# Optimization experiments

Measured on AMD Instinct MI355X. Metric: run time of the kernel, lower is better.

Reference implementation:

```python
import jax, jax.numpy as jnp
import numpy as np

D_MODEL = 1024
N_HEADS = 16
HEAD_DIM = D_MODEL // N_HEADS


def setup_inputs() -> dict:
    key = jax.random.key(0)
    ks = jax.random.split(key, 5)
    B, S = 2, 2048
    x = jax.random.normal(ks[0], (B, S, D_MODEL), dtype=jnp.float32)
    # nn.Linear weights: [out_features, in_features]
    s_in = 1.0 / np.sqrt(D_MODEL)
    qkv_w = jax.random.uniform(ks[1], (3 * D_MODEL, D_MODEL), jnp.float32, -s_in, s_in)
    qkv_b = jax.random.uniform(ks[2], (3 * D_MODEL,), jnp.float32, -s_in, s_in)
    out_w = jax.random.uniform(ks[3], (D_MODEL, D_MODEL), jnp.float32, -s_in, s_in)
    out_b = jax.random.uniform(ks[4], (D_MODEL,), jnp.float32, -s_in, s_in)
    return {"x": x, "qkv_w": qkv_w, "qkv_b": qkv_b, "out_w": out_w, "out_b": out_b}


def reference(x, qkv_w, qkv_b, out_w, out_b):
    B, S, D = x.shape
    H, Hd = N_HEADS, HEAD_DIM
    scale = 1.0 / np.sqrt(Hd)
    qkv = jnp.einsum('bsd,ed->bse', x, qkv_w) + qkv_b  # [B,S,3D]
    qkv = qkv.reshape(B, S, 3, H, Hd)
    q = qkv[:, :, 0].transpose(0, 2, 1, 3)  # [B,H,S,Hd]
    k = qkv[:, :, 1].transpose(0, 2, 1, 3)
    v = qkv[:, :, 2].transpose(0, 2, 1, 3)
    scores = jnp.einsum('bhqd,bhkd->bhqk', q, k) * scale  # [B,H,S,S]
    causal = jnp.triu(jnp.ones((S, S), dtype=bool), k=1)
    scores = jnp.where(causal[None, None], -jnp.inf, scores)
    probs = jax.nn.softmax(scores, axis=-1)
    out = jnp.einsum('bhqk,bhkd->bhqd', probs, v)  # [B,H,S,Hd]
    out = out.transpose(0, 2, 1, 3).reshape(B, S, D)
    out = jnp.einsum('bsd,ed->bse', out, out_w) + out_b
    return out
```

## Files before the change

### kernel.cpp

```cpp
#include <hip/hip_runtime.h>
#include <hip/hip_bf16.h>

#define SEQ    2048
#define DMODEL 1024
#define NHEAD  16
#define HDIM   64
#define BATCH  2
#define NTOK   (BATCH * SEQ)

#define N_X   (NTOK * DMODEL)
#define N_WQ  (3 * DMODEL * DMODEL)
#define N_BQ  (3 * DMODEL)
#define N_WO  (DMODEL * DMODEL)
#define N_BO  (DMODEL)
#define N_CANON (N_X + N_WQ + N_BQ + N_WO + N_BO)

#define NEG_SENT (-1.0e30f)
#define QSCALE 0.1803368801111f

typedef __attribute__((ext_vector_type(8))) short short8;
typedef __attribute__((ext_vector_type(4))) short short4v;
typedef __attribute__((ext_vector_type(4))) float f32x4;

#define MFMA_BF16(A, B, C) __builtin_amdgcn_mfma_f32_16x16x32_bf16((A), (B), (C), 0, 0, 0)

static __device__ __forceinline__ short8 load8(const __hip_bfloat16* p) {
    return *(const short8*)p;
}

static __device__ __forceinline__ void async16(const void* g, void* l) {
    __builtin_amdgcn_global_load_lds(
        (const __attribute__((address_space(1))) unsigned int*)g,
        (__attribute__((address_space(3))) unsigned int*)l,
        16, 0, 0);
}

__global__ void detect_kernel(const unsigned short* __restrict__ w, int* flag) {
    int cnt = 0;
    for (int i = threadIdx.x; i < 512; i += 64) {
        const unsigned e = (w[i] >> 7) & 0xFF;
        if (e >= 125) cnt++;
    }
#pragma unroll
    for (int o = 32; o; o >>= 1) cnt += __shfl_down(cnt, o);
    if (threadIdx.x == 0) *flag = (cnt > 8) ? 1 : 0;
}

__global__ __launch_bounds__(256) void canon_kernel(
    const void* __restrict__ s0, const void* __restrict__ s1,
    const void* __restrict__ s2, const void* __restrict__ s3,
    const void* __restrict__ s4,
    __hip_bfloat16* __restrict__ dst, const int* __restrict__ flag)
{
    const int idx = blockIdx.x * 256 + threadIdx.x;
    if (idx >= N_CANON) return;
    const void* src;
    int off;
    if (idx < N_X)                         { src = s0; off = idx; }
    else if (idx < N_X + N_WQ)             { src = s1; off = idx - N_X; }
    else if (idx < N_X + N_WQ + N_BQ)      { src = s2; off = idx - (N_X + N_WQ); }
    else if (idx < N_X + N_WQ + N_BQ + N_WO){ src = s3; off = idx - (N_X + N_WQ + N_BQ); }
    else                                   { src = s4; off = idx - (N_X + N_WQ + N_BQ + N_WO); }
    const bool isf32 = (*flag != 0);
    const float v = isf32 ? ((const float*)src)[off]
                          : __bfloat162float(((const __hip_bfloat16*)src)[off]);
    dst[idx] = __float2bfloat16(v);
}

__global__ __launch_bounds__(256) void qkv_gemm_kernel(
    const __hip_bfloat16* __restrict__ X,
    const __hip_bfloat16* __restrict__ W,
    const __hip_bfloat16* __restrict__ bias,
    __hip_bfloat16* __restrict__ Qs,
    __hip_bfloat16* __restrict__ Kb,
    __hip_bfloat16* __restrict__ Vt)
{
    constexpr int Kd = DMODEL;
    __shared__ __align__(16) __hip_bfloat16 As[128 * 32];
    __shared__ __align__(16) __hip_bfloat16 Bs[128 * 32];

    const int tid   = threadIdx.x;
    const int lane  = tid & 63;
    const int w     = tid >> 6;
    const int mTile = blockIdx.y * 128;
    const int nTile = blockIdx.x * 128;
    const int wm    = (w >> 1) * 64;
    const int wn    = (w & 1) * 64;
    const int lm    = lane & 15;
    const int lk    = (lane >> 4) * 8;

    f32x4 acc[4][4];
#pragma unroll
    for (int i = 0; i < 4; ++i)
#pragma unroll
        for (int j = 0; j < 4; ++j)
            acc[i][j] = (f32x4){0.f, 0.f, 0.f, 0.f};

    const int r0c = tid >> 2, p0c = tid & 3;
    const int r1c = (tid + 256) >> 2, p1c = tid & 3;

    for (int k0 = 0; k0 < Kd; k0 += 32) {
        __syncthreads();
        async16(&X[(size_t)(mTile + r0c) * Kd + k0 + p0c * 8], (char*)As + tid * 16);
        async16(&X[(size_t)(mTile + r1c) * Kd + k0 + p1c * 8], (char*)As + tid * 16 + 4096);
        async16(&W[(size_t)(nTile + r0c) * Kd + k0 + p0c * 8], (char*)Bs + tid * 16);
        async16(&W[(size_t)(nTile + r1c) * Kd + k0 + p1c * 8], (char*)Bs + tid * 16 + 4096);
        __syncthreads();

        short8 a[4], b[4];
#pragma unroll
        for (int i = 0; i < 4; ++i)
            a[i] = *(const short8*)&As[(wm + i * 16 + lm) * 32 + lk];
#pragma unroll
        for (int j = 0; j < 4; ++j)
            b[j] = *(const short8*)&Bs[(wn + j * 16 + lm) * 32 + lk];
#pragma unroll
        for (int i = 0; i < 4; ++i)
#pragma unroll
            for (int j = 0; j < 4; ++j)
                acc[i][j] = MFMA_BF16(a[i], b[j], acc[i][j]);
    }

    const int r0 = (lane >> 4) * 4;
#pragma unroll
    for (int j = 0; j < 4; ++j) {
        const int n  = nTile + wn + j * 16 + lm;
        const float bv = __bfloat162float(bias[n]);
        const int c = n >> 10;
        const int h = (n >> 6) & 15;
        const int d = n & 63;
#pragma unroll
        for (int i = 0; i < 4; ++i) {
#pragma unroll
            for (int r = 0; r < 4; ++r) {
                const int m  = mTile + wm + i * 16 + r0 + r;
                const int bb = m >> 11;
                const int s  = m & (SEQ - 1);
                const int bh = bb * NHEAD + h;
                const float v = acc[i][j][r] + bv;
                if (c == 0) {
                    Qs[(size_t)(bh * SEQ + s) * HDIM + d] = __float2bfloat16(v * QSCALE);
                } else if (c == 1) {
                    Kb[(size_t)(bh * SEQ + s) * HDIM + d] = __float2bfloat16(v);
                } else {
                    Vt[(size_t)(bh * HDIM + d) * SEQ + s] = __float2bfloat16(v);
                }
            }
        }
    }
}

#define P_PITCH 72
__global__ __launch_bounds__(256, 2) void attn_kernel(
    const __hip_bfloat16* __restrict__ Qs,
    const __hip_bfloat16* __restrict__ Kb,
    const __hip_bfloat16* __restrict__ Vt,
    __hip_bfloat16* __restrict__ O)
{
    __shared__ __align__(16) __hip_bfloat16 Kt[64 * 64];
    __shared__ __align__(16) __hip_bfloat16 Vs[64 * 64];
    __shared__ __align__(16) __hip_bfloat16 Pall[4][32 * P_PITCH];

    const int lane = threadIdx.x & 63;
    const int wv   = threadIdx.x >> 6;
    const int pr   = blockIdx.x;
    const int bh   = blockIdx.y;

    const int lm  = lane & 15;
    const int q4  = lane >> 4;
    const int lk  = q4 * 8;
    const int swz = (lm & 3) << 4;

    __hip_bfloat16* P = Pall[wv];

    const __hip_bfloat16* Qbh = Qs + (size_t)bh * SEQ * HDIM;
    const __hip_bfloat16* Kbh = Kb + (size_t)bh * SEQ * HDIM;
    const __hip_bfloat16* Vbh = Vt + (size_t)bh * HDIM * SEQ;

    const int srow = (lane >> 3);
    const int scb  = (lane & 7) ^ srow;
    const int krow0 = wv * 16 + srow;
    const int krow1 = wv * 16 + 8 + srow;

    const int b  = bh >> 4;
    const int hh = bh & 15;

    for (int ph = 0; ph < 2; ++ph) {
        const int qb    = ph ? pr : 15 - pr;
        const int qbase = qb * 128;
        const int wbase = qbase + wv * 32;

        short8 qa[2][2];
#pragma unroll
        for (int i = 0; i < 2; ++i)
#pragma unroll
            for (int h = 0; h < 2; ++h)
                qa[i][h] = load8(&Qbh[(size_t)(wbase + i * 16 + lm) * HDIM + h * 32 + lk]);

        float m_run[2] = {NEG_SENT, NEG_SENT};
        float l_run[2] = {0.f, 0.f};
        f32x4 Oacc[2][4];
#pragma unroll
        for (int i = 0; i < 2; ++i)
#pragma unroll
            for (int t = 0; t < 4; ++t) Oacc[i][t] = (f32x4){0.f, 0.f, 0.f, 0.f};

        const int nChunks = 2 * (qb + 1);
        for (int c = 0; c < nChunks; ++c) {
            const int k0 = c * 64;

            __syncthreads();
            async16(&Kbh[(size_t)(k0 + krow0) * HDIM + scb * 8],
                    (char*)Kt + (size_t)(wv * 16) * 128 + (lane * 16));
            async16(&Kbh[(size_t)(k0 + krow1) * HDIM + scb * 8],
                    (char*)Kt + (size_t)(wv * 16 + 8) * 128 + (lane * 16));
            async16(&Vbh[(size_t)krow0 * SEQ + k0 + scb * 8],
                    (char*)Vs + (size_t)(wv * 16) * 128 + (lane * 16));
            async16(&Vbh[(size_t)krow1 * SEQ + k0 + scb * 8],
                    (char*)Vs + (size_t)(wv * 16 + 8) * 128 + (lane * 16));
            __syncthreads();

            if (k0 <= wbase + 31) {
                short8 ka[4][2];
#pragma unroll
                for (int t = 0; t < 4; ++t)
#pragma unroll
                    for (int h = 0; h < 2; ++h)
                        ka[t][h] = *(const short8*)&Kt[(t * 16 + lm) * 64 +
                                                       (((h * 4 + q4) ^ (lm & 7)) * 8)];

                f32x4 sc[2][4];
#pragma unroll
                for (int i = 0; i < 2; ++i)
#pragma unroll
                    for (int t = 0; t < 4; ++t) sc[i][t] = (f32x4){0.f, 0.f, 0.f, 0.f};
#pragma unroll
                for (int t = 0; t < 4; ++t)
#pragma unroll
                    for (int i = 0; i < 2; ++i) {
                        sc[i][t] = MFMA_BF16(ka[t][0], qa[i][0], sc[i][t]);
                        sc[i][t] = MFMA_BF16(ka[t][1], qa[i][1], sc[i][t]);
                    }

                if (k0 + 63 > wbase) {
#pragma unroll
                    for (int i = 0; i < 2; ++i) {
                        const int row = wbase + i * 16 + lm;
#pragma unroll
                        for (int t = 0; t < 4; ++t)
#pragma unroll
                            for (int r = 0; r < 4; ++r) {
                                const int key = k0 + t * 16 + q4 * 4 + r;
                                if (key > row) sc[i][t][r] = NEG_SENT;
                            }
                    }
                }

                float alpha[2];
#pragma unroll
                for (int i = 0; i < 2; ++i) {
                    float mx = sc[i][0][0];
#pragma unroll
                    for (int t = 0; t < 4; ++t)
#pragma unroll
                        for (int r = 0; r < 4; ++r) mx = fmaxf(mx, sc[i][t][r]);
                    mx = fmaxf(mx, __shfl_xor(mx, 16));
                    mx = fmaxf(mx, __shfl_xor(mx, 32));
                    const float mn = fmaxf(m_run[i], mx);
                    alpha[i] = exp2f(m_run[i] - mn);
                    float s = 0.f;
#pragma unroll
                    for (int t = 0; t < 4; ++t)
#pragma unroll
                        for (int r = 0; r < 4; ++r) {
                            const float p = exp2f(sc[i][t][r] - mn);
                            sc[i][t][r] = p;
                            s += p;
                        }
                    s += __shfl_xor(s, 16);
                    s += __shfl_xor(s, 32);
                    l_run[i] = l_run[i] * alpha[i] + s;
                    m_run[i] = mn;
                }

#pragma unroll
                for (int i = 0; i < 2; ++i)
#pragma unroll
                    for (int r = 0; r < 4; ++r) {
                        const float av = __shfl(alpha[i], q4 * 4 + r);
#pragma unroll
                        for (int t = 0; t < 4; ++t) Oacc[i][t][r] *= av;
                    }

#pragma unroll
                for (int i = 0; i < 2; ++i)
#pragma unroll
                    for (int t = 0; t < 4; ++t) {
                        short4v pk;
#pragma unroll
                        for (int r = 0; r < 4; ++r)
                            pk[r] = (short)__bfloat16_as_ushort(__float2bfloat16(sc[i][t][r]));
                        const int col = (t * 16 + q4 * 4) ^ swz;
                        *(short4v*)&P[(i * 16 + lm) * P_PITCH + col] = pk;
                    }

#pragma unroll
                for (int h = 0; h < 2; ++h) {
                    short8 pa[2];
#pragma unroll
                    for (int i = 0; i < 2; ++i) {
                        const int col = (h * 32 + lk) ^ swz;
                        pa[i] = *(const short8*)&P[(i * 16 + lm) * P_PITCH + col];
                    }
#pragma unroll
                    for (int t = 0; t < 4; ++t) {
                        const short8 vb = *(const short8*)&Vs[(t * 16 + lm) * 64 +
                                                              (((h * 4 + q4) ^ (lm & 7)) * 8)];
#pragma unroll
                        for (int i = 0; i < 2; ++i)
                            Oacc[i][t] = MFMA_BF16(pa[i], vb, Oacc[i][t]);
                    }
                }
            }
        }

#pragma unroll
        for (int i = 0; i < 2; ++i)
#pragma unroll
            for (int r = 0; r < 4; ++r) {
                const float lv = __shfl(l_run[i], q4 * 4 + r);
                const float inv = 1.0f / lv;
                const size_t m = (size_t)b * SEQ + wbase + i * 16 + q4 * 4 + r;
#pragma unroll
                for (int t = 0; t < 4; ++t)
                    O[m * DMODEL + hh * 64 + t * 16 + lm] = __float2bfloat16(Oacc[i][t][r] * inv);
            }
    }
}

__global__ __launch_bounds__(256) void proj_gemm_kernel(
    const __hip_bfloat16* __restrict__ A,
    const __hip_bfloat16* __restrict__ W,
    const __hip_bfloat16* __restrict__ bias,
    void* __restrict__ outv,
    const int* __restrict__ flag)
{
    constexpr int Kd = DMODEL;
    __shared__ __align__(16) __hip_bfloat16 As[128 * 32];
    __shared__ __align__(16) __hip_bfloat16 Bs[128 * 32];

    const int tid   = threadIdx.x;
    const int lane  = tid & 63;
    const int w     = tid >> 6;
    const int mTile = blockIdx.y * 128;
    const int nTile = blockIdx.x * 128;
    const int wm    = (w >> 1) * 64;
    const int wn    = (w & 1) * 64;
    const int lm    = lane & 15;
    const int lk    = (lane >> 4) * 8;
    const bool f32out = (*flag != 0);

    f32x4 acc[4][4];
#pragma unroll
    for (int i = 0; i < 4; ++i)
#pragma unroll
        for (int j = 0; j < 4; ++j)
            acc[i][j] = (f32x4){0.f, 0.f, 0.f, 0.f};

    const int r0c = tid >> 2, p0c = tid & 3;
    const int r1c = (tid + 256) >> 2, p1c = tid & 3;

    for (int k0 = 0; k0 < Kd; k0 += 32) {
        __syncthreads();
        async16(&A[(size_t)(mTile + r0c) * Kd + k0 + p0c * 8], (char*)As + tid * 16);
        async16(&A[(size_t)(mTile + r1c) * Kd + k0 + p1c * 8], (char*)As + tid * 16 + 4096);
        async16(&W[(size_t)(nTile + r0c) * Kd + k0 + p0c * 8], (char*)Bs + tid * 16);
        async16(&W[(size_t)(nTile + r1c) * Kd + k0 + p1c * 8], (char*)Bs + tid * 16 + 4096);
        __syncthreads();

        short8 a[4], b[4];
#pragma unroll
        for (int i = 0; i < 4; ++i)
            a[i] = *(const short8*)&As[(wm + i * 16 + lm) * 32 + lk];
#pragma unroll
        for (int j = 0; j < 4; ++j)
            b[j] = *(const short8*)&Bs[(wn + j * 16 + lm) * 32 + lk];
#pragma unroll
        for (int i = 0; i < 4; ++i)
#pragma unroll
            for (int j = 0; j < 4; ++j)
                acc[i][j] = MFMA_BF16(a[i], b[j], acc[i][j]);
    }

    const int r0 = (lane >> 4) * 4;
#pragma unroll
    for (int j = 0; j < 4; ++j) {
        const int n = nTile + wn + j * 16 + lm;
        const float bv = __bfloat162float(bias[n]);
#pragma unroll
        for (int i = 0; i < 4; ++i) {
#pragma unroll
            for (int r = 0; r < 4; ++r) {
                const size_t m = mTile + wm + i * 16 + r0 + r;
                const float v = acc[i][j][r] + bv;
                if (f32out) ((float*)outv)[m * DMODEL + n] = v;
                else ((__hip_bfloat16*)outv)[m * DMODEL + n] = __float2bfloat16(v);
            }
        }
    }
}

extern "C" void kernel_launch(void* const* d_in, const int* in_sizes, int n_in,
                              void* d_out, int out_size, void* d_ws, size_t ws_size,
                              hipStream_t stream) {
    const size_t OFF_CANON = 256;
    const size_t OFF_QS = OFF_CANON + (size_t)N_CANON * 2;
    const size_t OFF_KB = OFF_QS + (size_t)NTOK * DMODEL * 2;
    const size_t OFF_VT = OFF_KB + (size_t)NTOK * DMODEL * 2;
    const size_t OFF_AO = OFF_VT + (size_t)NTOK * DMODEL * 2;

    char* wsb = (char*)d_ws;
    int* flag = (int*)wsb;
    __hip_bfloat16* canon = (__hip_bfloat16*)(wsb + OFF_CANON);
    __hip_bfloat16* Xc = canon;
    __hip_bfloat16* Wq = Xc + N_X;
    __hip_bfloat16* Bq = Wq + N_WQ;
    __hip_bfloat16* Wo = Bq + N_BQ;
    __hip_bfloat16* Bo = Wo + N_WO;
    __hip_bfloat16* Qs = (__hip_bfloat16*)(wsb + OFF_QS);
    __hip_bfloat16* Kb = (__hip_bfloat16*)(wsb + OFF_KB);
    __hip_bfloat16* Vt = (__hip_bfloat16*)(wsb + OFF_VT);
    __hip_bfloat16* Ao = (__hip_bfloat16*)(wsb + OFF_AO);

    detect_kernel<<<1, 64, 0, stream>>>((const unsigned short*)d_in[1], flag);
    canon_kernel<<<(N_CANON + 255) / 256, 256, 0, stream>>>(
        d_in[0], d_in[1], d_in[2], d_in[3], d_in[4], canon, flag);

    {
        dim3 grid(3 * DMODEL / 128, NTOK / 128);
        qkv_gemm_kernel<<<grid, 256, 0, stream>>>(Xc, Wq, Bq, Qs, Kb, Vt);
    }
    {
        dim3 grid(8, BATCH * NHEAD);
        attn_kernel<<<grid, 256, 0, stream>>>(Qs, Kb, Vt, Ao);
    }
    {
        dim3 grid(DMODEL / 128, NTOK / 128);
        proj_gemm_kernel<<<grid, 256, 0, stream>>>(Ao, Wo, Bo, d_out, flag);
    }
}
```

Baseline: 232.4 us.

## Double-buffer K/V tiles and split attention block into eight 16-row waves

The attention kernel now runs 512 threads (8 waves), each wave handling 16 query rows instead of 32. K/V tiles are double-buffered in shared memory, with the next chunk's async loads issued before computing on the current one, using explicit vmcnt waits and raw barriers. This is meant to hide global-load latency and raise wave-level parallelism. In exchange, each wave reuses its K/V fragments across fewer rows, shared memory use grows, and the hand-written waitcnt and barrier sequencing adds fragility.

```diff
diff --git a/kernel.cpp b/kernel.cpp
--- a/kernel.cpp
+++ b/kernel.cpp
@@ -151,18 +151,19 @@
 }
 
 #define P_PITCH 72
-__global__ __launch_bounds__(256, 2) void attn_kernel(
+__global__ __launch_bounds__(512, 2) void attn_kernel(
     const __hip_bfloat16* __restrict__ Qs,
     const __hip_bfloat16* __restrict__ Kb,
     const __hip_bfloat16* __restrict__ Vt,
     __hip_bfloat16* __restrict__ O)
 {
-    __shared__ __align__(16) __hip_bfloat16 Kt[64 * 64];
-    __shared__ __align__(16) __hip_bfloat16 Vs[64 * 64];
-    __shared__ __align__(16) __hip_bfloat16 Pall[4][32 * P_PITCH];
-
-    const int lane = threadIdx.x & 63;
-    const int wv   = threadIdx.x >> 6;
+    __shared__ __align__(16) __hip_bfloat16 Kt[2][64 * 64];
+    __shared__ __align__(16) __hip_bfloat16 Vs[2][64 * 64];
+    __shared__ __align__(16) __hip_bfloat16 Pall[8][16 * P_PITCH];
+
+    const int tid  = threadIdx.x;
+    const int lane = tid & 63;
+    const int wv   = tid >> 6;
     const int pr   = blockIdx.x;
     const int bh   = blockIdx.y;
 
@@ -177,164 +178,146 @@
     const __hip_bfloat16* Kbh = Kb + (size_t)bh * SEQ * HDIM;
     const __hip_bfloat16* Vbh = Vt + (size_t)bh * HDIM * SEQ;
 
-    const int srow = (lane >> 3);
-    const int scb  = (lane & 7) ^ srow;
-    const int krow0 = wv * 16 + srow;
-    const int krow1 = wv * 16 + 8 + srow;
+    const int srow = tid >> 3;
+    const int scb  = (tid & 7) ^ (srow & 7);
 
     const int b  = bh >> 4;
     const int hh = bh & 15;
 
     for (int ph = 0; ph < 2; ++ph) {
         const int qb    = ph ? pr : 15 - pr;
-        const int qbase = qb * 128;
-        const int wbase = qbase + wv * 32;
-
-        short8 qa[2][2];
-#pragma unroll
-        for (int i = 0; i < 2; ++i)
-#pragma unroll
-            for (int h = 0; h < 2; ++h)
-                qa[i][h] = load8(&Qbh[(size_t)(wbase + i * 16 + lm) * HDIM + h * 32 + lk]);
-
-        float m_run[2] = {NEG_SENT, NEG_SENT};
-        float l_run[2] = {0.f, 0.f};
-        f32x4 Oacc[2][4];
-#pragma unroll
-        for (int i = 0; i < 2; ++i)
-#pragma unroll
-            for (int t = 0; t < 4; ++t) Oacc[i][t] = (f32x4){0.f, 0.f, 0.f, 0.f};
+        const int wbase = qb * 128 + wv * 16;
+
+        short8 qa[2];
+#pragma unroll
+        for (int h = 0; h < 2; ++h)
+            qa[h] = load8(&Qbh[(size_t)(wbase + lm) * HDIM + h * 32 + lk]);
+
+        float m_run = NEG_SENT;
+        float l_run = 0.f;
+        f32x4 Oacc[4];
+#pragma unroll
+        for (int t = 0; t < 4; ++t) Oacc[t] = (f32x4){0.f, 0.f, 0.f, 0.f};
 
         const int nChunks = 2 * (qb + 1);
+        int cur = 0;
+
+        async16(&Kbh[(size_t)srow * HDIM + scb * 8], (char*)Kt[0] + tid * 16);
+        async16(&Vbh[(size_t)srow * SEQ + scb * 8],  (char*)Vs[0] + tid * 16);
+
         for (int c = 0; c < nChunks; ++c) {
             const int k0 = c * 64;
 
-            __syncthreads();
-            async16(&Kbh[(size_t)(k0 + krow0) * HDIM + scb * 8],
-                    (char*)Kt + (size_t)(wv * 16) * 128 + (lane * 16));
-            async16(&Kbh[(size_t)(k0 + krow1) * HDIM + scb * 8],
-                    (char*)Kt + (size_t)(wv * 16 + 8) * 128 + (lane * 16));
-            async16(&Vbh[(size_t)krow0 * SEQ + k0 + scb * 8],
-                    (char*)Vs + (size_t)(wv * 16) * 128 + (lane * 16));
-            async16(&Vbh[(size_t)krow1 * SEQ + k0 + scb * 8],
-                    (char*)Vs + (size_t)(wv * 16 + 8) * 128 + (lane * 16));
-            __syncthreads();
-
-            if (k0 <= wbase + 31) {
+            if (c + 1 < nChunks) {
+                const int k1 = k0 + 64;
+                async16(&Kbh[(size_t)(k1 + srow) * HDIM + scb * 8],
+                        (char*)Kt[cur ^ 1] + tid * 16);
+                async16(&Vbh[(size_t)srow * SEQ + k1 + scb * 8],
+                        (char*)Vs[cur ^ 1] + tid * 16);
+                asm volatile("s_waitcnt vmcnt(2)" ::: "memory");
+            } else {
+                asm volatile("s_waitcnt vmcnt(0)" ::: "memory");
+            }
+            __builtin_amdgcn_s_barrier();
+            __builtin_amdgcn_sched_barrier(0);
+
+            if (k0 <= wbase + 15) {
+                const __hip_bfloat16* Kc = Kt[cur];
+                const __hip_bfloat16* Vc = Vs[cur];
+
                 short8 ka[4][2];
 #pragma unroll
                 for (int t = 0; t < 4; ++t)
 #pragma unroll
                     for (int h = 0; h < 2; ++h)
-                        ka[t][h] = *(const short8*)&Kt[(t * 16 + lm) * 64 +
+                        ka[t][h] = *(const short8*)&Kc[(t * 16 + lm) * 64 +
                                                        (((h * 4 + q4) ^ (lm & 7)) * 8)];
 
-                f32x4 sc[2][4];
-#pragma unroll
-                for (int i = 0; i < 2; ++i)
-#pragma unroll
-                    for (int t = 0; t < 4; ++t) sc[i][t] = (f32x4){0.f, 0.f, 0.f, 0.f};
+                f32x4 sc[4];
+#pragma unroll
+                for (int t = 0; t < 4; ++t) sc[t] = (f32x4){0.f, 0.f, 0.f, 0.f};
+#pragma unroll
+                for (int t = 0; t < 4; ++t) {
+                    sc[t] = MFMA_BF16(ka[t][0], qa[0], sc[t]);
+                    sc[t] = MFMA_BF16(ka[t][1], qa[1], sc[t]);
+                }
+
+                if (k0 + 63 > wbase) {
+                    const int row = wbase + lm;
+#pragma unroll
+                    for (int t = 0; t < 4; ++t)
+#pragma unroll
+                        for (int r = 0; r < 4; ++r) {
+                            const int key = k0 + t * 16 + q4 * 4 + r;
+                            if (key > row) sc[t][r] = NEG_SENT;
+                        }
+                }
+
+                float mx = sc[0][0];
 #pragma unroll
                 for (int t = 0; t < 4; ++t)
 #pragma unroll
-                    for (int i = 0; i < 2; ++i) {
-                        sc[i][t] = MFMA_BF16(ka[t][0], qa[i][0], sc[i][t]);
-                        sc[i][t] = MFMA_BF16(ka[t][1], qa[i][1], sc[i][t]);
+                    for (int r = 0; r < 4; ++r) mx = fmaxf(mx, sc[t][r]);
+                mx = fmaxf(mx, __shfl_xor(mx, 16));
+                mx = fmaxf(mx, __shfl_xor(mx, 32));
+                const float mn = fmaxf(m_run, mx);
+                const float alpha = exp2f(m_run - mn);
+                float s = 0.f;
+#pragma unroll
+                for (int t = 0; t < 4; ++t)
+#pragma unroll
+                    for (int r = 0; r < 4; ++r) {
+                        const float p = exp2f(sc[t][r] - mn);
+                        sc[t][r] = p;
+                        s += p;
                     }
-
-                if (k0 + 63 > wbase) {
-#pragma unroll
-                    for (int i = 0; i < 2; ++i) {
-                        const int row = wbase + i * 16 + lm;
-#pragma unroll
-                        for (int t = 0; t < 4; ++t)
-#pragma unroll
-                            for (int r = 0; r < 4; ++r) {
-                                const int key = k0 + t * 16 + q4 * 4 + r;
-                                if (key > row) sc[i][t][r] = NEG_SENT;
-                            }
+                s += __shfl_xor(s, 16);
+                s += __shfl_xor(s, 32);
+                l_run = l_run * alpha + s;
+                m_run = mn;
+
+#pragma unroll
+                for (int r = 0; r < 4; ++r) {
+                    const float av = __shfl(alpha, q4 * 4 + r);
+#pragma unroll
+                    for (int t = 0; t < 4; ++t) Oacc[t][r] *= av;
+                }
+
+#pragma unroll
+                for (int t = 0; t < 4; ++t) {
+                    short4v pk;
+#pragma unroll
+                    for (int r = 0; r < 4; ++r)
+                        pk[r] = (short)__bfloat16_as_ushort(__float2bfloat16(sc[t][r]));
+                    const int col = (t * 16 + q4 * 4) ^ swz;
+                    *(short4v*)&P[lm * P_PITCH + col] = pk;
+                }
+
+#pragma unroll
+                for (int h = 0; h < 2; ++h) {
+                    const short8 pa = *(const short8*)&P[lm * P_PITCH + ((h * 32 + lk) ^ swz)];
+#pragma unroll
+                    for (int t = 0; t < 4; ++t) {
+                        const short8 vb = *(const short8*)&Vc[(t * 16 + lm) * 64 +
+                                                              (((h * 4 + q4) ^ (lm & 7)) * 8)];
+                        Oacc[t] = MFMA_BF16(pa, vb, Oacc[t]);
                     }
                 }
-
-                float alpha[2];
-#pragma unroll
-                for (int i = 0; i < 2; ++i) {
-                    float mx = sc[i][0][0];
-#pragma unroll
-                    for (int t = 0; t < 4; ++t)
-#pragma unroll
-                        for (int r = 0; r < 4; ++r) mx = fmaxf(mx, sc[i][t][r]);
-                    mx = fmaxf(mx, __shfl_xor(mx, 16));
-                    mx = fmaxf(mx, __shfl_xor(mx, 32));
-                    const float mn = fmaxf(m_run[i], mx);
-                    alpha[i] = exp2f(m_run[i] - mn);
-                    float s = 0.f;
-#pragma unroll
-                    for (int t = 0; t < 4; ++t)
-#pragma unroll
-                        for (int r = 0; r < 4; ++r) {
-                            const float p = exp2f(sc[i][t][r] - mn);
-                            sc[i][t][r] = p;
-                            s += p;
-                        }
-                    s += __shfl_xor(s, 16);
-                    s += __shfl_xor(s, 32);
-                    l_run[i] = l_run[i] * alpha[i] + s;
-                    m_run[i] = mn;
-                }
-
-#pragma unroll
-                for (int i = 0; i < 2; ++i)
-#pragma unroll
-                    for (int r = 0; r < 4; ++r) {
-                        const float av = __shfl(alpha[i], q4 * 4 + r);
-#pragma unroll
-                        for (int t = 0; t < 4; ++t) Oacc[i][t][r] *= av;
-                    }
-
-#pragma unroll
-                for (int i = 0; i < 2; ++i)
-#pragma unroll
-                    for (int t = 0; t < 4; ++t) {
-                        short4v pk;
-#pragma unroll
-                        for (int r = 0; r < 4; ++r)
-                            pk[r] = (short)__bfloat16_as_ushort(__float2bfloat16(sc[i][t][r]));
-                        const int col = (t * 16 + q4 * 4) ^ swz;
-                        *(short4v*)&P[(i * 16 + lm) * P_PITCH + col] = pk;
-                    }
-
-#pragma unroll
-                for (int h = 0; h < 2; ++h) {
-                    short8 pa[2];
-#pragma unroll
-                    for (int i = 0; i < 2; ++i) {
-                        const int col = (h * 32 + lk) ^ swz;
-                        pa[i] = *(const short8*)&P[(i * 16 + lm) * P_PITCH + col];
-                    }
-#pragma unroll
-                    for (int t = 0; t < 4; ++t) {
-                        const short8 vb = *(const short8*)&Vs[(t * 16 + lm) * 64 +
-                                                              (((h * 4 + q4) ^ (lm & 7)) * 8)];
-#pragma unroll
-                        for (int i = 0; i < 2; ++i)
-                            Oacc[i][t] = MFMA_BF16(pa[i], vb, Oacc[i][t]);
-                    }
-                }
             }
+
+            __builtin_amdgcn_s_barrier();
+            cur ^= 1;
         }
 
 #pragma unroll
-        for (int i = 0; i < 2; ++i)
-#pragma unroll
-            for (int r = 0; r < 4; ++r) {
-                const float lv = __shfl(l_run[i], q4 * 4 + r);
-                const float inv = 1.0f / lv;
-                const size_t m = (size_t)b * SEQ + wbase + i * 16 + q4 * 4 + r;
-#pragma unroll
-                for (int t = 0; t < 4; ++t)
-                    O[m * DMODEL + hh * 64 + t * 16 + lm] = __float2bfloat16(Oacc[i][t][r] * inv);
-            }
+        for (int r = 0; r < 4; ++r) {
+            const float lv = __shfl(l_run, q4 * 4 + r);
+            const float inv = 1.0f / lv;
+            const size_t m = (size_t)b * SEQ + wbase + q4 * 4 + r;
+#pragma unroll
+            for (int t = 0; t < 4; ++t)
+                O[m * DMODEL + hh * 64 + t * 16 + lm] = __float2bfloat16(Oacc[t][r] * inv);
+        }
     }
 }
 
@@ -442,7 +425,7 @@
     }
     {
         dim3 grid(8, BATCH * NHEAD);
-        attn_kernel<<<grid, 256, 0, stream>>>(Qs, Kb, Vt, Ao);
+        attn_kernel<<<grid, 512, 0, stream>>>(Qs, Kb, Vt, Ao);
     }
     {
         dim3 grid(DMODEL / 128, NTOK / 128);
```

After: 218.5 us. 1.06x faster.
